# Optimization experiments

Hardware: AMD Instinct MI355X
Metric: run time of the kernel (lower is better)

Reference implementation:

```python
import jax, jax.numpy as jnp
import numpy as np

N_MOTIF_PER_CLASS = 8
N_CLASS = 16
N_MOTIF = N_MOTIF_PER_CLASS * N_CLASS
TEMPERATURE = 0.2
TAU = 0.99
K2 = 32
EPS = 1e-4


def setup_inputs() -> dict:
    key = jax.random.key(0)
    k1, k2, k3 = jax.random.split(key, 3)
    N, H = 32768, 1024
    z = jax.random.normal(k1, (N, H), dtype=jnp.float32)
    Motif_Vector = jax.random.normal(k2, (N_MOTIF, H), dtype=jnp.float32)
    y = jax.random.randint(k3, (N,), 0, N_CLASS, dtype=jnp.int64)
    return {"z": z, "Motif_Vector": Motif_Vector, "y": y}


def euclidean_1(X, M):
    # squared euclidean distance via GEMM, then log-ratio similarity
    xp = X @ M.T                                     # [N, n_motif]
    distance = (-2.0 * xp
                + jnp.sum(X * X, axis=1, keepdims=True)
                + jnp.sum(M * M, axis=1)[None, :])
    similarity = jnp.log((distance + 1.0) / (distance + EPS))
    return similarity, distance


def reference(z, Motif_Vector, y):
    similarity, distance = euclidean_1(z, Motif_Vector)

    # mapping: motif j belongs to class j // n_motif_per_class
    motif_class = jnp.arange(N_MOTIF) // N_MOTIF_PER_CLASS   # [n_motif]
    true_motifs = (y[:, None] == motif_class[None, :])       # [N, n_motif]

    # contrastive loss (exact torch math: exp(sim/T), max over positives,
    # sum over negatives)
    sims = jnp.exp(similarity / TEMPERATURE)
    sim_pos = jnp.max(jnp.where(true_motifs, sims, -jnp.inf), axis=1)
    sim_neg_sum = jnp.sum(jnp.where(true_motifs, 0.0, sims), axis=1)
    loss = -jnp.mean(jnp.log(sim_pos / (sim_neg_sum + sim_pos)))

    # update_motif (update_type='topk', weighted_mean=False):
    # torch passes `distance` into filter_similar_graph and argsorts
    # descending, i.e. selects the K2 LARGEST distances among same-class
    # samples (faithful to source).
    masked = jnp.where(true_motifs.T, distance.T, -jnp.inf)  # [n_motif, N]
    _, idx = jax.lax.top_k(masked, K2)                       # [n_motif, K2]
    selected = z[idx]                                        # [n_motif, K2, H]
    new_motif = jnp.mean(selected, axis=1)                   # weights = 1/K2
    new_M = TAU * Motif_Vector + (1.0 - TAU) * new_motif

    return loss, new_M
```

## Files before the change

### kernel.cpp

```cpp
#include <hip/hip_runtime.h>
#include <cstdint>
#include <cmath>

#define NROWS 32768
#define HD    1024
#define NMOT  128
#define NCLS  16
#define KSEL  32
#define EPSV  1e-4f

typedef __attribute__((ext_vector_type(4))) float  f32x4;
typedef __attribute__((ext_vector_type(8))) __bf16 bf16x8;
typedef __attribute__((ext_vector_type(4))) __bf16 bf16x4;
typedef unsigned long long u64;

#define WS_LP   0
#define WS_MN   512
#define WS_MVBF 1024
#define WS_S1K  66560
#define WS_CD   197632
#define CAPC    256

static __device__ __forceinline__ float dot4(float4 v) {
    return v.x * v.x + v.y * v.y + v.z * v.z + v.w * v.w;
}
static __device__ __forceinline__ float dot4v(f32x4 v) {
    return v[0] * v[0] + v[1] * v[1] + v[2] * v[2] + v[3] * v[3];
}

static __device__ __forceinline__ bf16x4 cvt4(float4 v) {
    bf16x4 t;
    t[0] = (__bf16)v.x; t[1] = (__bf16)v.y; t[2] = (__bf16)v.z; t[3] = (__bf16)v.w;
    return t;
}

static __device__ __forceinline__ bf16x8 cvt8v(f32x4 a, f32x4 b) {
    bf16x8 t;
    t[0] = (__bf16)a[0]; t[1] = (__bf16)a[1]; t[2] = (__bf16)a[2]; t[3] = (__bf16)a[3];
    t[4] = (__bf16)b[0]; t[5] = (__bf16)b[1]; t[6] = (__bf16)b[2]; t[7] = (__bf16)b[3];
    return t;
}

static __device__ __forceinline__ void gl16(const void* g, void* l) {
    __builtin_amdgcn_global_load_lds(
        (const __attribute__((address_space(1))) void*)g,
        (__attribute__((address_space(3))) void*)l, 16, 0, 0);
}

#define LOADA(dst, base, imm)                                        \
    asm volatile("global_load_dwordx4 %0, %1, off offset:%2"         \
                 : "=&v"(dst) : "v"(base), "n"(imm))

#define WAITN(n) asm volatile("s_waitcnt vmcnt(" #n ")" ::: "memory")

static __device__ __forceinline__ u64 pack_key(float v, int idx) {
    unsigned int b = __float_as_uint(v);
    unsigned int mo = (b & 0x80000000u) ? ~b : (b | 0x80000000u);
    unsigned int khi = ~mo;
    return ((u64)khi << 32) | (unsigned int)idx;
}

__global__ __launch_bounds__(256) void prep_k(const float* __restrict__ mv,
                                              float* __restrict__ mn,
                                              __bf16* __restrict__ mvbf) {
    const int b = blockIdx.x;
    const int tid = threadIdx.x;
    const int k = tid * 4;
    float4 v = *(const float4*)&mv[(size_t)b * HD + k];
    *(bf16x4*)&mvbf[(size_t)b * HD + k] = cvt4(v);
    float s = dot4(v);
#pragma unroll
    for (int o = 1; o < 64; o <<= 1) s += __shfl_xor(s, o, 64);
    __shared__ float red[4];
    if ((tid & 63) == 0) red[tid >> 6] = s;
    __syncthreads();
    if (tid == 0) mn[b] = red[0] + red[1] + red[2] + red[3];
}

#define BK 32
#define NS 32
#define SPC 8

__global__ __launch_bounds__(512, 1) void gemm_fused(
    const float* __restrict__ z, const __bf16* __restrict__ mvbf,
    const float* __restrict__ mn, float* __restrict__ cd,
    const int* __restrict__ y, float* __restrict__ lossP) {
    __shared__ __align__(16) __bf16 Bs[2][32768];
    __shared__ float redw[8];

    const int tid  = threadIdx.x;
    const int lane = tid & 63;
    const int wid  = tid >> 6;
    const int l15  = lane & 15;
    const int quad = lane >> 4;
    const int rg   = blockIdx.x;
    const int myrow = rg * 128 + wid * 16 + l15;

    const float* zb = z + (size_t)myrow * HD + quad * 8;

    char* bs0 = (char*)Bs[0];
    char* bs1 = (char*)Bs[1];

#pragma unroll
    for (int i = 0; i < 8; ++i)
        gl16(mvbf + (size_t)(i * 16 + l15) * HD + wid * 32 + quad * 8,
             bs0 + (wid * 8 + i) * 1024);

    f32x4 ra[4][2];
#pragma unroll
    for (int s = 0; s < 4; ++s) {
        LOADA(ra[s][0], zb, s * 128);
        LOADA(ra[s][1], zb, s * 128 + 16);
    }
    WAITN(6);
    __builtin_amdgcn_sched_barrier(0);
    __builtin_amdgcn_s_barrier();
    asm volatile("" ::: "memory");

    f32x4 acc[8];
#pragma unroll
    for (int j = 0; j < 8; ++j) acc[j] = (f32x4){0.f, 0.f, 0.f, 0.f};
    float zsq = 0.f;

#pragma unroll
    for (int kc = 0; kc < 4; ++kc) {
        const char* bsc = ((kc & 1) ? bs1 : bs0) + lane * 16;
        if (kc + 1 < 4) {
            char* bsn = (((kc + 1) & 1) ? bs1 : bs0);
#pragma unroll
            for (int i = 0; i < 8; ++i)
                gl16(mvbf + (size_t)(i * 16 + l15) * HD + (kc + 1) * 256 +
                         wid * 32 + quad * 8,
                     bsn + (wid * 8 + i) * 1024);
        }
#pragma unroll
        for (int m = 0; m < SPC; ++m) {
            const int kt = kc * SPC + m;
            if (kc < 3) {
                if (m < 4) WAITN(14); else WAITN(6);
            } else {
                if (m <= 4) WAITN(6);
                else if (m == 5) WAITN(4);
                else if (m == 6) WAITN(2);
                else WAITN(0);
            }
            __builtin_amdgcn_sched_barrier(0);

            bf16x8 bfr[8];
#pragma unroll
            for (int j = 0; j < 8; ++j)
                bfr[j] = *(const bf16x8*)(bsc + (m * 8 + j) * 1024);

            const int sl = kt & 3;
            zsq += dot4v(ra[sl][0]) + dot4v(ra[sl][1]);
            bf16x8 af = cvt8v(ra[sl][0], ra[sl][1]);
            if (kt + 4 < NS) {
                LOADA(ra[sl][0], zb, (kt + 4) * 128);
                LOADA(ra[sl][1], zb, (kt + 4) * 128 + 16);
            }
#pragma unroll
            for (int j = 0; j < 8; ++j)
                acc[j] = __builtin_amdgcn_mfma_f32_16x16x32_bf16(
                    af, bfr[j], acc[j], 0, 0, 0);
        }
        if (kc < 3) {
            asm volatile("s_waitcnt lgkmcnt(0)" ::: "memory");
            __builtin_amdgcn_s_barrier();
            asm volatile("" ::: "memory");
            __builtin_amdgcn_sched_barrier(0);
        }
    }

    zsq += __shfl_xor(zsq, 16, 64);
    zsq += __shfl_xor(zsq, 32, 64);
    const int yv = y[myrow];
    float mcv[8];
#pragma unroll
    for (int j = 0; j < 8; ++j) mcv[j] = mn[j * 16 + l15];

    float znv[4]; int rcls[4];
#pragma unroll
    for (int reg = 0; reg < 4; ++reg) {
        znv[reg]  = __shfl(zsq, quad * 4 + reg, 64);
        rcls[reg] = __shfl(yv,  quad * 4 + reg, 64);
    }
    float pm[4], ns[4];
#pragma unroll
    for (int reg = 0; reg < 4; ++reg) { pm[reg] = 0.f; ns[reg] = 0.f; }

#pragma unroll
    for (int j = 0; j < 8; ++j) {
        const int c = j * 16 + l15;
        const float mc = mcv[j];
        const int ccls = c >> 3;
#pragma unroll
        for (int reg = 0; reg < 4; ++reg) {
            float d = znv[reg] + mc - 2.f * acc[j][reg];
            float r = (d + 1.0f) * __builtin_amdgcn_rcpf(d + EPSV);
            float r2 = r * r;
            float s = r2 * r2 * r;
            if (ccls == rcls[reg]) {
                pm[reg] = fmaxf(pm[reg], s);
                const int row = rg * 128 + wid * 16 + quad * 4 + reg;
                cd[(size_t)row * 8 + (c & 7)] = d;
            } else {
                ns[reg] += s;
            }
        }
    }
#pragma unroll
    for (int o = 1; o < 16; o <<= 1)
#pragma unroll
        for (int reg = 0; reg < 4; ++reg) {
            pm[reg] = fmaxf(pm[reg], __shfl_xor(pm[reg], o, 64));
            ns[reg] += __shfl_xor(ns[reg], o, 64);
        }
    float li = 0.f;
    if (l15 == 0) {
#pragma unroll
        for (int reg = 0; reg < 4; ++reg)
            li += logf((ns[reg] + pm[reg]) / pm[reg]);
    }
    li += __shfl_xor(li, 16, 64);
    li += __shfl_xor(li, 32, 64);
    if (lane == 0) redw[wid] = li;
    __syncthreads();
    if (tid == 0) {
        float t = 0.f;
#pragma unroll
        for (int w = 0; w < 8; ++w) t += redw[w];
        lossP[blockIdx.x] = t;
    }
}

__global__ __launch_bounds__(256) void sel1_k(const int* __restrict__ y,
                                              const float* __restrict__ cd,
                                              u64* __restrict__ s1k) {
    __shared__ u64 keys[256];
    __shared__ int clist[CAPC];
    __shared__ int cnt;

    const int bid = blockIdx.x;
    const int j = bid >> 4, chunk = bid & 15;
    const int cls = j >> 3, m8 = j & 7;
    const int tid = threadIdx.x;
    const int lane = tid & 63;

    if (tid == 0) cnt = 0;
    __syncthreads();
    const int base = chunk * 2048;
#pragma unroll
    for (int t = 0; t < 8; ++t) {
        const int i = base + t * 256 + tid;
        const bool pred = (y[i] == cls);
        const u64 m = __ballot(pred);
        int wbase = 0;
        if (lane == 0 && m) wbase = atomicAdd(&cnt, (int)__popcll(m));
        wbase = __shfl(wbase, 0, 64);
        if (pred) {
            const int p = wbase + (int)__popcll(m & ((1ull << lane) - 1ull));
            if (p < CAPC) clist[p] = i;
        }
    }
    __syncthreads();
    const int n = cnt < CAPC ? cnt : CAPC;

    u64 key = ~0ull;
    if (tid < n) {
        const int idx = clist[tid];
        key = pack_key(cd[(size_t)idx * 8 + m8], idx);
    }
    keys[tid] = key;
    __syncthreads();

    for (int k = 2; k <= 256; k <<= 1) {
        for (int jj = k >> 1; jj > 0; jj >>= 1) {
            if (tid < 128) {
                const int i  = ((tid & ~(jj - 1)) << 1) | (tid & (jj - 1));
                const int ix = i | jj;
                const u64 A = keys[i], B = keys[ix];
                const bool up = ((i & k) == 0);
                if ((A > B) == up) { keys[i] = B; keys[ix] = A; }
            }
            __syncthreads();
        }
    }
    if (tid < KSEL) s1k[(size_t)j * 512 + chunk * KSEL + tid] = keys[tid];
}

__global__ __launch_bounds__(256) void merge_k(
    const float* __restrict__ z, const float* __restrict__ mv,
    const u64* __restrict__ s1k, const float* __restrict__ lossP,
    float* __restrict__ out) {
    __shared__ u64 keys[512];
    __shared__ int sel[KSEL];
    __shared__ float redf[4];

    const int b = blockIdx.x;
    const int j = b >> 2, q = b & 3;
    const int tid = threadIdx.x;
    const int lane = tid & 63;
    const int wave = tid >> 6;

    if (b == 0) {
        float s = lossP[tid];
#pragma unroll
        for (int o = 1; o < 64; o <<= 1) s += __shfl_xor(s, o, 64);
        if (lane == 0) redf[wave] = s;
        __syncthreads();
        if (tid == 0)
            out[0] = (redf[0] + redf[1] + redf[2] + redf[3]) * (1.0f / NROWS);
    }

    keys[tid]       = s1k[(size_t)j * 512 + tid];
    keys[tid + 256] = s1k[(size_t)j * 512 + 256 + tid];
    __syncthreads();

    for (int k = 2; k <= 512; k <<= 1) {
        for (int jj = k >> 1; jj > 0; jj >>= 1) {
            const int i  = ((tid & ~(jj - 1)) << 1) | (tid & (jj - 1));
            const int ix = i | jj;
            const u64 A = keys[i], B = keys[ix];
            const bool up = ((i & k) == 0);
            if ((A > B) == up) { keys[i] = B; keys[ix] = A; }
            __syncthreads();
        }
    }
    if (tid < KSEL) sel[tid] = (int)(keys[tid] & 0xFFFFFFFFu);
    __syncthreads();

    const int h = q * 256 + tid;
    float s = 0.f;
#pragma unroll 8
    for (int r = 0; r < KSEL; ++r) s += z[(size_t)sel[r] * HD + h];
    out[1 + (size_t)j * HD + h] =
        0.99f * mv[(size_t)j * HD + h] + 0.01f * (s * (1.0f / KSEL));
}

extern "C" void kernel_launch(void* const* d_in, const int* in_sizes, int n_in,
                              void* d_out, int out_size, void* d_ws, size_t ws_size,
                              hipStream_t stream) {
    const float* z  = (const float*)d_in[0];
    const float* mv = (const float*)d_in[1];
    const int*   y  = (const int*)d_in[2];
    float* out = (float*)d_out;
    float* wsf = (float*)d_ws;
    float*  lossP = wsf + WS_LP;
    float*  mn    = wsf + WS_MN;
    __bf16* mvbf  = (__bf16*)(wsf + WS_MVBF);
    u64*    s1k   = (u64*)(wsf + WS_S1K);
    float*  cd    = wsf + WS_CD;

    hipLaunchKernelGGL(prep_k,     dim3(NMOT),      dim3(256), 0, stream,
                       mv, mn, mvbf);
    hipLaunchKernelGGL(gemm_fused, dim3(256),       dim3(512), 0, stream,
                       z, mvbf, mn, cd, y, lossP);
    hipLaunchKernelGGL(sel1_k,     dim3(NMOT * 16), dim3(256), 0, stream,
                       y, cd, s1k);
    hipLaunchKernelGGL(merge_k,    dim3(NMOT * 4),  dim3(256), 0, stream,
                       z, mv, s1k, lossP, out);
}
```

Baseline: 233.0 us.

## Retile fused GEMM into smaller 32-row blocks with 2x2 waves for occupancy

The fused distance/loss GEMM moves from 256 blocks of 512 threads (128 rows each, 128 KB LDS, one block per CU) to 1024 blocks of 256 threads covering 32 rows. The four waves form a 2x2 grid over rows and motif columns, and motifs are staged in 64-wide K chunks with 32 KB of LDS, so up to four blocks can share a CU. The aim is to fill all CUs (256 blocks underfill a 256-CU part) and hide latency through occupancy. The costs are 16 barriers instead of 4, z rows now loaded twice (once per column wave), and a cross-wave LDS reduction of the max/sum terms. Workspace offsets and the loss partial reduction are resized for 1024 partials.

Result: slower. 239.4 us (+2.7%).

```diff
diff --git a/kernel.cpp b/kernel.cpp
--- a/kernel.cpp
+++ b/kernel.cpp
@@ -15,10 +15,10 @@
 typedef unsigned long long u64;
 
 #define WS_LP   0
-#define WS_MN   512
-#define WS_MVBF 1024
-#define WS_S1K  66560
-#define WS_CD   197632
+#define WS_MN   1024
+#define WS_MVBF 2048
+#define WS_S1K  34816
+#define WS_CD   165888
 #define CAPC    256
 
 static __device__ __forceinline__ float dot4(float4 v) {
@@ -79,33 +79,41 @@
 
 #define BK 32
 #define NS 32
-#define SPC 8
-
-__global__ __launch_bounds__(512, 1) void gemm_fused(
+#define NCH 16
+
+__global__ __launch_bounds__(256, 4) void gemm_fused(
     const float* __restrict__ z, const __bf16* __restrict__ mvbf,
     const float* __restrict__ mn, float* __restrict__ cd,
     const int* __restrict__ y, float* __restrict__ lossP) {
-    __shared__ __align__(16) __bf16 Bs[2][32768];
-    __shared__ float redw[8];
+    __shared__ __align__(16) __bf16 Bs[2][8192];
+    __shared__ float sns[2][32];
+    __shared__ float spm[2][32];
 
     const int tid  = threadIdx.x;
     const int lane = tid & 63;
     const int wid  = tid >> 6;
+    const int wr   = wid >> 1;
+    const int wc   = wid & 1;
     const int l15  = lane & 15;
     const int quad = lane >> 4;
-    const int rg   = blockIdx.x;
-    const int myrow = rg * 128 + wid * 16 + l15;
+    const int rb   = blockIdx.x * 32;
+    const int myrow = rb + wr * 16 + l15;
 
     const float* zb = z + (size_t)myrow * HD + quad * 8;
 
-    char* bs0 = (char*)Bs[0];
-    char* bs1 = (char*)Bs[1];
-
-#pragma unroll
-    for (int i = 0; i < 8; ++i)
-        gl16(mvbf + (size_t)(i * 16 + l15) * HD + wid * 32 + quad * 8,
-             bs0 + (wid * 8 + i) * 1024);
-
+#define STAGE(kc, buf)                                                        \
+    {                                                                         \
+        _Pragma("unroll")                                                     \
+        for (int i = 0; i < 4; ++i) {                                         \
+            const int g = wid * 4 + i;                                        \
+            const int jj = g & 7, ss = g >> 3;                                \
+            gl16(mvbf + (size_t)(jj * 16 + l15) * HD + (kc) * 64 + ss * 32 +  \
+                     quad * 8,                                                \
+                 (char*)Bs[buf] + g * 1024);                                  \
+        }                                                                     \
+    }
+
+    STAGE(0, 0);
     f32x4 ra[4][2];
 #pragma unroll
     for (int s = 0; s < 4; ++s) {
@@ -117,39 +125,33 @@
     __builtin_amdgcn_s_barrier();
     asm volatile("" ::: "memory");
 
-    f32x4 acc[8];
-#pragma unroll
-    for (int j = 0; j < 8; ++j) acc[j] = (f32x4){0.f, 0.f, 0.f, 0.f};
+    f32x4 acc[4];
+#pragma unroll
+    for (int j = 0; j < 4; ++j) acc[j] = (f32x4){0.f, 0.f, 0.f, 0.f};
     float zsq = 0.f;
 
 #pragma unroll
-    for (int kc = 0; kc < 4; ++kc) {
-        const char* bsc = ((kc & 1) ? bs1 : bs0) + lane * 16;
-        if (kc + 1 < 4) {
-            char* bsn = (((kc + 1) & 1) ? bs1 : bs0);
-#pragma unroll
-            for (int i = 0; i < 8; ++i)
-                gl16(mvbf + (size_t)(i * 16 + l15) * HD + (kc + 1) * 256 +
-                         wid * 32 + quad * 8,
-                     bsn + (wid * 8 + i) * 1024);
-        }
-#pragma unroll
-        for (int m = 0; m < SPC; ++m) {
-            const int kt = kc * SPC + m;
-            if (kc < 3) {
-                if (m < 4) WAITN(14); else WAITN(6);
+    for (int kc = 0; kc < NCH; ++kc) {
+        if (kc + 1 < NCH) STAGE(kc + 1, (kc + 1) & 1);
+        const char* bsc = (const char*)Bs[kc & 1] + lane * 16;
+#pragma unroll
+        for (int m = 0; m < 2; ++m) {
+            const int kt = kc * 2 + m;
+            if (m == 0) {
+                if (kc == 0) WAITN(10);
+                else if (kc == NCH - 1) WAITN(6);
+                else WAITN(14);
             } else {
-                if (m <= 4) WAITN(6);
-                else if (m == 5) WAITN(4);
-                else if (m == 6) WAITN(2);
-                else WAITN(0);
+                if (kc == NCH - 2) WAITN(0);
+                else if (kc == NCH - 1) WAITN(4);
+                else WAITN(2);
             }
             __builtin_amdgcn_sched_barrier(0);
 
-            bf16x8 bfr[8];
-#pragma unroll
-            for (int j = 0; j < 8; ++j)
-                bfr[j] = *(const bf16x8*)(bsc + (m * 8 + j) * 1024);
+            bf16x8 bfr[4];
+#pragma unroll
+            for (int j = 0; j < 4; ++j)
+                bfr[j] = *(const bf16x8*)(bsc + (m * 8 + wc * 4 + j) * 1024);
 
             const int sl = kt & 3;
             zsq += dot4v(ra[sl][0]) + dot4v(ra[sl][1]);
@@ -159,11 +161,11 @@
                 LOADA(ra[sl][1], zb, (kt + 4) * 128 + 16);
             }
 #pragma unroll
-            for (int j = 0; j < 8; ++j)
+            for (int j = 0; j < 4; ++j)
                 acc[j] = __builtin_amdgcn_mfma_f32_16x16x32_bf16(
                     af, bfr[j], acc[j], 0, 0, 0);
         }
-        if (kc < 3) {
+        if (kc + 1 < NCH) {
             asm volatile("s_waitcnt lgkmcnt(0)" ::: "memory");
             __builtin_amdgcn_s_barrier();
             asm volatile("" ::: "memory");
@@ -174,9 +176,6 @@
     zsq += __shfl_xor(zsq, 16, 64);
     zsq += __shfl_xor(zsq, 32, 64);
     const int yv = y[myrow];
-    float mcv[8];
-#pragma unroll
-    for (int j = 0; j < 8; ++j) mcv[j] = mn[j * 16 + l15];
 
     float znv[4]; int rcls[4];
 #pragma unroll
@@ -189,9 +188,9 @@
     for (int reg = 0; reg < 4; ++reg) { pm[reg] = 0.f; ns[reg] = 0.f; }
 
 #pragma unroll
-    for (int j = 0; j < 8; ++j) {
-        const int c = j * 16 + l15;
-        const float mc = mcv[j];
+    for (int j = 0; j < 4; ++j) {
+        const int c = wc * 64 + j * 16 + l15;
+        const float mc = mn[c];
         const int ccls = c >> 3;
 #pragma unroll
         for (int reg = 0; reg < 4; ++reg) {
@@ -201,7 +200,7 @@
             float s = r2 * r2 * r;
             if (ccls == rcls[reg]) {
                 pm[reg] = fmaxf(pm[reg], s);
-                const int row = rg * 128 + wid * 16 + quad * 4 + reg;
+                const int row = rb + wr * 16 + quad * 4 + reg;
                 cd[(size_t)row * 8 + (c & 7)] = d;
             } else {
                 ns[reg] += s;
@@ -215,21 +214,25 @@
             pm[reg] = fmaxf(pm[reg], __shfl_xor(pm[reg], o, 64));
             ns[reg] += __shfl_xor(ns[reg], o, 64);
         }
-    float li = 0.f;
     if (l15 == 0) {
 #pragma unroll
-        for (int reg = 0; reg < 4; ++reg)
-            li += logf((ns[reg] + pm[reg]) / pm[reg]);
-    }
-    li += __shfl_xor(li, 16, 64);
-    li += __shfl_xor(li, 32, 64);
-    if (lane == 0) redw[wid] = li;
-    __syncthreads();
-    if (tid == 0) {
-        float t = 0.f;
-#pragma unroll
-        for (int w = 0; w < 8; ++w) t += redw[w];
-        lossP[blockIdx.x] = t;
+        for (int reg = 0; reg < 4; ++reg) {
+            const int rloc = wr * 16 + quad * 4 + reg;
+            spm[wc][rloc] = pm[reg];
+            sns[wc][rloc] = ns[reg];
+        }
+    }
+    __syncthreads();
+    if (tid < 64) {
+        float li = 0.f;
+        if (tid < 32) {
+            const float p = fmaxf(spm[0][tid], spm[1][tid]);
+            const float nsum = sns[0][tid] + sns[1][tid];
+            li = logf((nsum + p) / p);
+        }
+#pragma unroll
+        for (int o = 1; o < 64; o <<= 1) li += __shfl_xor(li, o, 64);
+        if (tid == 0) lossP[blockIdx.x] = li;
     }
 }
 
@@ -303,7 +306,8 @@
     const int wave = tid >> 6;
 
     if (b == 0) {
-        float s = lossP[tid];
+        float s = lossP[tid] + lossP[tid + 256] + lossP[tid + 512] +
+                  lossP[tid + 768];
 #pragma unroll
         for (int o = 1; o < 64; o <<= 1) s += __shfl_xor(s, o, 64);
         if (lane == 0) redf[wave] = s;
@@ -353,7 +357,7 @@
 
     hipLaunchKernelGGL(prep_k,     dim3(NMOT),      dim3(256), 0, stream,
                        mv, mn, mvbf);
-    hipLaunchKernelGGL(gemm_fused, dim3(256),       dim3(512), 0, stream,
+    hipLaunchKernelGGL(gemm_fused, dim3(1024),      dim3(256), 0, stream,
                        z, mvbf, mn, cd, y, lossP);
     hipLaunchKernelGGL(sel1_k,     dim3(NMOT * 16), dim3(256), 0, stream,
                        y, cd, s1k);
```
